# Performance work log

Measured on AMD Instinct MI355X. Metric: run time of the kernel, lower is better.

Reference implementation:

```python
import jax, jax.numpy as jnp
import numpy as np

GRID_SIZE = 5
SPLINE_ORDER = 3
NUM_BASIS = GRID_SIZE + SPLINE_ORDER  # 8


def _make_grid(in_features):
    # efficient-kan style uniform extended grid over [-1, 1]
    h = 2.0 / GRID_SIZE
    g = jnp.arange(-SPLINE_ORDER, GRID_SIZE + SPLINE_ORDER + 1, dtype=jnp.float32) * h - 1.0
    return jnp.broadcast_to(g, (in_features, g.shape[0]))  # [in, 12]


def _b_splines(x, grid):
    # x: [..., in], grid: [in, G]; returns [..., in, NUM_BASIS] via Cox-de Boor
    xe = x[..., None]
    bases = ((xe >= grid[:, :-1]) & (xe < grid[:, 1:])).astype(x.dtype)
    for k in range(1, SPLINE_ORDER + 1):
        left = (xe - grid[:, :-(k + 1)]) / (grid[:, k:-1] - grid[:, :-(k + 1)]) * bases[..., :-1]
        right = (grid[:, k + 1:] - xe) / (grid[:, k + 1:] - grid[:, 1:-k]) * bases[..., 1:]
        bases = left + right
    return bases


def kan_linear(x, bw, sw):
    # bw: [out, in], sw: [out, in, NUM_BASIS]
    base = jnp.matmul(jax.nn.silu(x), bw.T)
    spl = _b_splines(x, _make_grid(bw.shape[1]))
    spline = jnp.einsum('...ik,oik->...o', spl, sw)
    return base + spline


def kan2(x, bw1, sw1, bw2, sw2):
    return kan_linear(kan_linear(x, bw1, sw1), bw2, sw2)


def _att_matrix(q, bw1, sw1, bw2, sw2):
    n, h = q.shape
    pairs = jnp.concatenate([
        jnp.broadcast_to(q[:, None, :], (n, n, h)),
        jnp.broadcast_to(q[None, :, :], (n, n, h)),
    ], axis=-1)  # [n, n, 2h]
    return kan2(pairs, bw1, sw1, bw2, sw2)[..., 0]  # [n, n]


def setup_inputs() -> dict:
    key = jax.random.key(0)
    ks = jax.random.split(key, 32)
    n, h, m = 384, 32, 50

    def rn(k, shape, s=1.0):
        return jax.random.normal(k, shape, dtype=jnp.float32) * s

    inp = {
        'x': rn(ks[0], (n, h)),
        'y': rn(ks[1], (n, h)),
        'target': rn(ks[2], (n, h)),
        'bias': rn(ks[3], (1,), 0.1),
    }
    i = 4
    for pre in ('x', 'y', 't'):
        din = 2 * h
        inp[pre + '1bw'] = rn(ks[i], (m, din), 0.1)
        inp[pre + '1sw'] = rn(ks[i + 1], (m, din, NUM_BASIS), 0.1)
        inp[pre + '2bw'] = rn(ks[i + 2], (1, m), 0.1)
        inp[pre + '2sw'] = rn(ks[i + 3], (1, m, NUM_BASIS), 0.1)
        i += 4
    inp['f1bw'] = rn(ks[i], (m, 3 * h), 0.1)
    inp['f1sw'] = rn(ks[i + 1], (m, 3 * h, NUM_BASIS), 0.1)
    inp['f2bw'] = rn(ks[i + 2], (3, m), 0.1)
    inp['f2sw'] = rn(ks[i + 3], (3, m, NUM_BASIS), 0.1)
    i += 4
    inp['l1bw'] = rn(ks[i], (h, h), 0.1)
    inp['l1sw'] = rn(ks[i + 1], (h, h, NUM_BASIS), 0.1)
    inp['l2bw'] = rn(ks[i + 2], (h, h), 0.1)
    inp['l2sw'] = rn(ks[i + 3], (h, h, NUM_BASIS), 0.1)
    return inp


def reference(x, y, target, bias,
              x1bw, x1sw, x2bw, x2sw,
              y1bw, y1sw, y2bw, y2sw,
              t1bw, t1sw, t2bw, t2sw,
              f1bw, f1sw, f2bw, f2sw,
              l1bw, l1sw, l2bw, l2sw):
    xA = _att_matrix(x, x1bw, x1sw, x2bw, x2sw)
    yA = _att_matrix(y, y1bw, y1sw, y2bw, y2sw)
    tA = _att_matrix(target, t1bw, t1sw, t2bw, t2sw)

    # dynamic modal fusion weights
    feats = jnp.concatenate([x.mean(0, keepdims=True), y.mean(0, keepdims=True),
                             target.mean(0, keepdims=True)], axis=-1)  # [1, 3h]
    w = jax.nn.softmax(kan2(feats, f1bw, f1sw, f2bw, f2sw), axis=-1)[0]  # [3]

    fusion_att = w[0] * xA + w[1] * yA + w[2] * tA + bias
    fusion_att = jax.nn.softmax(fusion_att, axis=-1)
    target_att = jnp.matmul(fusion_att, target)  # dropout is identity at eval
    y1 = jax.nn.relu(kan_linear(target_att, l1bw, l1sw))
    y2 = jax.nn.relu(kan_linear(y1, l2bw, l2sw))
    return y2
```

## Files before the change

kernel.cpp:

```cpp
#include <hip/hip_runtime.h>

#define NN 384
#define HH 32
#define MM 50

__device__ __forceinline__ float fastRcp(float x) { return __builtin_amdgcn_rcpf(x); }

__device__ __forceinline__ void featEval(float x, float& sil, int& kb, float b[4]) {
  sil = x * fastRcp(1.0f + __expf(-x));
  const float u  = (x + 1.0f) * 2.5f;
  const float fu = floorf(u);
  const bool valid = (fu >= -3.0f) && (fu <= 7.0f);
  const float s = valid ? (1.0f / 6.0f) : 0.0f;
  kb = valid ? (int)fu : 100;
  const float tt = u - fu;
  const float t2 = tt * tt, t3 = t2 * tt, omt = 1.0f - tt;
  b[0] = omt * omt * omt * s;
  b[1] = (3.0f * t3 - 6.0f * t2 + 4.0f) * s;
  b[2] = (-3.0f * t3 + 3.0f * t2 + 3.0f * tt + 1.0f) * s;
  b[3] = t3 * s;
}

__device__ __forceinline__ float waveReduce(float v) {
#pragma unroll
  for (int off = 32; off > 0; off >>= 1) v += __shfl_down(v, off);
  return v;
}

__device__ __forceinline__ float dot4(float4 a, float4 b) {
  float r = a.x * b.x;
  r = fmaf(a.y, b.y, r);
  r = fmaf(a.z, b.z, r);
  r = fmaf(a.w, b.w, r);
  return r;
}

__global__ __launch_bounds__(384) void stageA_kernel(
    const float* __restrict__ x, const float* __restrict__ y, const float* __restrict__ tg,
    const float* __restrict__ xbw, const float* __restrict__ xsw,
    const float* __restrict__ ybw, const float* __restrict__ ysw,
    const float* __restrict__ tbw, const float* __restrict__ tsw,
    const float* __restrict__ f1bw, const float* __restrict__ f1sw,
    const float* __restrict__ f2bw, const float* __restrict__ f2sw,
    float* __restrict__ A, float* __restrict__ Bt, float* __restrict__ wout)
{
  const int tid = threadIdx.x;
  const int lane = tid & 63, w = tid >> 6;
  const int i = blockIdx.x;
  const int m = blockIdx.y;
  const int half = blockIdx.z;

  if (i < NN) {
    __shared__ float bas[HH * 8];
    __shared__ float sil[HH];
    const float* q  = (m == 0) ? x   : ((m == 1) ? y   : tg);
    const float* bw = (m == 0) ? xbw : ((m == 1) ? ybw : tbw);
    const float* sw = (m == 0) ? xsw : ((m == 1) ? ysw : tsw);
    const int cb = half * HH;

    if (tid < HH * 8) bas[tid] = 0.0f;
    __syncthreads();
    if (tid < HH) {
      float b[4]; float s; int kb;
      featEval(q[i * HH + tid], s, kb, b);
      sil[tid] = s;
#pragma unroll
      for (int r = 0; r < 4; ++r) {
        const int k = kb + r;
        if ((unsigned)k < 8u) bas[tid * 8 + k] = b[r];
      }
    }
    __syncthreads();

    const float4* bas4 = (const float4*)bas;
    const float4 bb = bas4[lane];
    const float sl = (lane < HH) ? sil[lane] : 0.0f;
#pragma unroll 2
    for (int o = w; o < MM; o += 6) {
      const float4 wv4 = ((const float4*)(sw + ((size_t)(o * 2 * HH + cb) << 3)))[lane];
      const float bwv = (lane < HH) ? bw[o * 2 * HH + cb + lane] : 0.0f;
      float acc = dot4(wv4, bb);
      acc = fmaf(bwv, sl, acc);
      acc = waveReduce(acc);
      if (lane == 0) {
        if (half == 0) A[((size_t)m * NN + i) * MM + o] = acc;
        else           Bt[((size_t)m * MM + o) * NN + i] = acc;
      }
    }
    return;
  }

  if (m != 0 || half != 0) return;
  {
    __shared__ float4 part4[3][8][16];
    __shared__ float sil96[96];
    __shared__ float bas768[96 * 8];
    __shared__ float z1[MM];
    __shared__ float sil2[MM];
    __shared__ float bas400[MM * 8];
    __shared__ float s3[3];

    {
      const int mm = tid >> 7;
      const int sub = tid & 127;
      const int q4 = sub >> 4;
      const int prt = sub & 15;
      const float* src = (mm == 0) ? x : ((mm == 1) ? y : tg);
      const float4* s4 = (const float4*)src;
      float4 a = make_float4(0.f, 0.f, 0.f, 0.f);
      for (int r = prt; r < NN; r += 16) {
        const float4 v = s4[r * 8 + q4];
        a.x += v.x; a.y += v.y; a.z += v.z; a.w += v.w;
      }
      part4[mm][q4][prt] = a;
    }
    for (int idx = tid; idx < 96 * 8; idx += 384) bas768[idx] = 0.0f;
    for (int idx = tid; idx < MM * 8; idx += 384) bas400[idx] = 0.0f;
    __syncthreads();

    if (tid < 96) {
      const int mm = tid >> 5, col = tid & 31;
      const int q4 = col >> 2, comp = col & 3;
      const float* pp = (const float*)&part4[mm][q4][0];
      float v = 0.0f;
#pragma unroll
      for (int prt = 0; prt < 16; ++prt) v += pp[prt * 4 + comp];
      const float fv = v * (1.0f / NN);
      float b[4]; float s; int kb;
      featEval(fv, s, kb, b);
      sil96[tid] = s;
#pragma unroll
      for (int r = 0; r < 4; ++r) {
        const int k = kb + r;
        if ((unsigned)k < 8u) bas768[tid * 8 + k] = b[r];
      }
    }
    __syncthreads();

    {
      const float4* bas4 = (const float4*)bas768;
      for (int o = w; o < MM; o += 6) {
        const float4* sp4 = (const float4*)(f1sw + (size_t)o * (96 * 8));
        float acc = 0.0f;
#pragma unroll
        for (int r = 0; r < 3; ++r)
          acc += dot4(sp4[lane + 64 * r], bas4[lane + 64 * r]);
#pragma unroll
        for (int r = 0; r < 2; ++r) {
          const int e = lane + 64 * r;
          if (e < 96) acc = fmaf(f1bw[o * 96 + e], sil96[e], acc);
        }
        acc = waveReduce(acc);
        if (lane == 0) z1[o] = acc;
      }
    }
    __syncthreads();

    if (tid < MM) {
      float b[4]; float s; int kb;
      featEval(z1[tid], s, kb, b);
      sil2[tid] = s;
#pragma unroll
      for (int r = 0; r < 4; ++r) {
        const int k = kb + r;
        if ((unsigned)k < 8u) bas400[tid * 8 + k] = b[r];
      }
    }
    __syncthreads();

    if (w < 3) {
      const float4* bas4 = (const float4*)bas400;
      const float4* sp4 = (const float4*)(f2sw + (size_t)w * (MM * 8));
      float acc = 0.0f;
#pragma unroll
      for (int r = 0; r < 2; ++r) {
        const int f = lane + 64 * r;
        if (f < MM * 2) acc += dot4(sp4[f], bas4[f]);
      }
      if (lane < MM) acc = fmaf(f2bw[w * MM + lane], sil2[lane], acc);
      acc = waveReduce(acc);
      if (lane == 0) s3[w] = acc;
    }
    __syncthreads();

    if (tid == 0) {
      const float mx = fmaxf(s3[0], fmaxf(s3[1], s3[2]));
      const float e0 = __expf(s3[0] - mx), e1 = __expf(s3[1] - mx), e2 = __expf(s3[2] - mx);
      const float inv = fastRcp(e0 + e1 + e2);
      wout[0] = e0 * inv; wout[1] = e1 * inv; wout[2] = e2 * inv;
    }
  }
}

__global__ __launch_bounds__(384) void score_kernel(
    const float* __restrict__ A, const float* __restrict__ Bt,
    const float* __restrict__ x2bw, const float* __restrict__ y2bw, const float* __restrict__ t2bw,
    const float* __restrict__ x2sw, const float* __restrict__ y2sw, const float* __restrict__ t2sw,
    float* __restrict__ Sp)
{
  __shared__ float sA[MM];
  __shared__ float sBW[MM];
  __shared__ float4 herm[43];
  __shared__ float4 coefC[MM][43];
  const int tid = threadIdx.x;
  const int i = blockIdx.x;
  const int m = blockIdx.y;
  const float* bsrc = (m == 0) ? x2bw : ((m == 1) ? y2bw : t2bw);
  const float* ssrc = (m == 0) ? x2sw : ((m == 1) ? y2sw : t2sw);

  if (tid < MM) {
    sA[tid]  = A[((size_t)m * NN + i) * MM + tid];
    sBW[tid] = bsrc[tid];
  }
  if (tid >= 64 && tid < 64 + 43) {
    const int c = tid - 64;
    float4 h;
    if (c == 0) {
      h = make_float4(0.f, 0.f, 0.f, 0.f);
    } else if (c == 42) {
      h = make_float4(8.2f, 0.4f, 0.f, 0.f);
    } else {
      const float z0 = -8.2f + (float)(c - 1) * 0.4f;
      const float z1 = z0 + 0.4f;
      const float s0 = fastRcp(1.0f + __expf(-z0));
      const float s1 = fastRcp(1.0f + __expf(-z1));
      const float p0 = z0 * s0, p1 = z1 * s1;
      const float m0 = 0.4f * (s0 * (1.0f + z0 * (1.0f - s0)));
      const float m1 = 0.4f * (s1 * (1.0f + z1 * (1.0f - s1)));
      h.x = p0;
      h.y = m0;
      h.z = 3.0f * (p1 - p0) - 2.0f * m0 - m1;
      h.w = 2.0f * (p0 - p1) + m0 + m1;
    }
    herm[c] = h;
  }
  __syncthreads();

  for (int idx = tid; idx < MM * 43; idx += 384) {
    const int k = idx / 43, cc = idx - k * 43;
    const float bwk = sBW[k];
    const float4 H = herm[cc];
    float4 C = make_float4(bwk * H.x, bwk * H.y, bwk * H.z, bwk * H.w);
    if (cc >= 16 && cc <= 26) {
      const int j = cc - 16;
      float p[4];
#pragma unroll
      for (int r = 0; r < 4; ++r) {
        const int pi = j + r - 3;
        p[r] = ((unsigned)pi < 8u) ? ssrc[k * 8 + pi] : 0.0f;
      }
      C.x += (p[0] + 4.0f * p[1] + p[2]) * (1.0f / 6.0f);
      C.y += (p[2] - p[0]) * 0.5f;
      C.z += (p[0] - 2.0f * p[1] + p[2]) * 0.5f;
      C.w += (p[3] - p[0]) * (1.0f / 6.0f) + (p[1] - p[2]) * 0.5f;
    }
    coefC[k][cc] = C;
  }
  __syncthreads();

#define KAN_EVAL(zz, kk, accv)                                          \
  {                                                                     \
    const float z_ = (zz);                                              \
    const float u_ = fmaf(z_, 2.5f, 20.5f);                             \
    const float fu_ = floorf(u_);                                       \
    const float cu_ = fminf(fmaxf(fu_, -1.0f), 41.0f);                  \
    const float t_ = u_ - cu_;                                          \
    const int cc_ = (int)cu_ + 1;                                       \
    const float4 C_ = coefC[kk][cc_];                                   \
    accv += fmaf(t_, fmaf(t_, fmaf(t_, C_.w, C_.z), C_.y), C_.x);       \
  }

  const float* BtBase = Bt + (size_t)m * MM * NN + tid;
  float acc0 = 0.0f, acc1 = 0.0f;
  float za = BtBase[0];
  float zb = BtBase[NN];
  float zc = BtBase[2 * NN];
  float zd = BtBase[3 * NN];
#pragma unroll 5
  for (int k = 0; k < MM; k += 2) {
    float ze = 0.0f, zf = 0.0f;
    if (k + 5 < MM) {
      ze = BtBase[(size_t)(k + 4) * NN];
      zf = BtBase[(size_t)(k + 5) * NN];
    }
    KAN_EVAL(sA[k] + za,     k,     acc0);
    KAN_EVAL(sA[k + 1] + zb, k + 1, acc1);
    za = zc; zb = zd; zc = ze; zd = zf;
  }
#undef KAN_EVAL

  Sp[((size_t)m * NN + i) * NN + tid] = acc0 + acc1;
}

__global__ __launch_bounds__(384) void row_kernel(
    const float* __restrict__ Sp, const float* __restrict__ wv, const float* __restrict__ bias,
    const float* __restrict__ tg,
    const float* __restrict__ l1bw, const float* __restrict__ l1sw,
    const float* __restrict__ l2bw, const float* __restrict__ l2sw,
    float* __restrict__ out)
{
  __shared__ float p[NN];
  __shared__ float redm[6], reds[6];
  __shared__ float part[12][HH];
  __shared__ float ta[HH];
  __shared__ float basF[HH * 8];
  __shared__ float silF[HH];
  __shared__ float y1v[HH];
  const int tid = threadIdx.x;
  const int lane = tid & 63, w = tid >> 6;
  const int i = blockIdx.x;

  float stot = bias[0];
  stot = fmaf(wv[0], Sp[(size_t)i * NN + tid], stot);
  stot = fmaf(wv[1], Sp[((size_t)NN + i) * NN + tid], stot);
  stot = fmaf(wv[2], Sp[((size_t)2 * NN + i) * NN + tid], stot);

  float v = stot;
#pragma unroll
  for (int off = 32; off > 0; off >>= 1) v = fmaxf(v, __shfl_down(v, off));
  if (lane == 0) redm[w] = v;
  __syncthreads();
  float mx = redm[0];
#pragma unroll
  for (int ww = 1; ww < 6; ++ww) mx = fmaxf(mx, redm[ww]);
  const float e = __expf(stot - mx);
  p[tid] = e;
  float sv = e;
#pragma unroll
  for (int off = 32; off > 0; off >>= 1) sv += __shfl_down(sv, off);
  if (lane == 0) reds[w] = sv;
  __syncthreads();
  const float ssum = reds[0] + reds[1] + reds[2] + reds[3] + reds[4] + reds[5];
  const float inv = 1.0f / ssum;

  const int d = tid & 31, g = tid >> 5;
  float acc2 = 0.0f;
  for (int s2 = 0; s2 < 32; ++s2) {
    const int j = g * 32 + s2;
    acc2 = fmaf(p[j], tg[j * HH + d], acc2);
  }
  part[g][d] = acc2;
  if (tid < HH * 8) basF[tid] = 0.0f;
  __syncthreads();
  if (tid < HH) {
    float a = 0.0f;
#pragma unroll
    for (int gg = 0; gg < 12; ++gg) a += part[gg][tid];
    ta[tid] = a * inv;
  }
  __syncthreads();

  if (tid < HH) {
    float b[4]; float s; int kb;
    featEval(ta[tid], s, kb, b);
    silF[tid] = s;
#pragma unroll
    for (int r = 0; r < 4; ++r) {
      const int k = kb + r;
      if ((unsigned)k < 8u) basF[tid * 8 + k] = b[r];
    }
  }
  __syncthreads();
  {
    const float4 bb = ((const float4*)basF)[lane];
    for (int o = w; o < HH; o += 6) {
      const float4* sp4 = (const float4*)(l1sw + ((size_t)o << 8));
      float acc = dot4(sp4[lane], bb);
      if (lane < HH) acc = fmaf(l1bw[o * HH + lane], silF[lane], acc);
      acc = waveReduce(acc);
      if (lane == 0) y1v[o] = fmaxf(acc, 0.0f);
    }
  }
  __syncthreads();
  if (tid < HH * 8) basF[tid] = 0.0f;
  __syncthreads();
  if (tid < HH) {
    float b[4]; float s; int kb;
    featEval(y1v[tid], s, kb, b);
    silF[tid] = s;
#pragma unroll
    for (int r = 0; r < 4; ++r) {
      const int k = kb + r;
      if ((unsigned)k < 8u) basF[tid * 8 + k] = b[r];
    }
  }
  __syncthreads();
  {
    const float4 bb = ((const float4*)basF)[lane];
    for (int o = w; o < HH; o += 6) {
      const float4* sp4 = (const float4*)(l2sw + ((size_t)o << 8));
      float acc = dot4(sp4[lane], bb);
      if (lane < HH) acc = fmaf(l2bw[o * HH + lane], silF[lane], acc);
      acc = waveReduce(acc);
      if (lane == 0) out[i * HH + o] = fmaxf(acc, 0.0f);
    }
  }
}

extern "C" void kernel_launch(void* const* d_in, const int* in_sizes, int n_in,
                              void* d_out, int out_size, void* d_ws, size_t ws_size,
                              hipStream_t stream)
{
  const float* x    = (const float*)d_in[0];
  const float* y    = (const float*)d_in[1];
  const float* tg   = (const float*)d_in[2];
  const float* bias = (const float*)d_in[3];
  const float* x1bw = (const float*)d_in[4];
  const float* x1sw = (const float*)d_in[5];
  const float* x2bw = (const float*)d_in[6];
  const float* x2sw = (const float*)d_in[7];
  const float* y1bw = (const float*)d_in[8];
  const float* y1sw = (const float*)d_in[9];
  const float* y2bw = (const float*)d_in[10];
  const float* y2sw = (const float*)d_in[11];
  const float* t1bw = (const float*)d_in[12];
  const float* t1sw = (const float*)d_in[13];
  const float* t2bw = (const float*)d_in[14];
  const float* t2sw = (const float*)d_in[15];
  const float* f1bw = (const float*)d_in[16];
  const float* f1sw = (const float*)d_in[17];
  const float* f2bw = (const float*)d_in[18];
  const float* f2sw = (const float*)d_in[19];
  const float* l1bw = (const float*)d_in[20];
  const float* l1sw = (const float*)d_in[21];
  const float* l2bw = (const float*)d_in[22];
  const float* l2sw = (const float*)d_in[23];
  float* out = (float*)d_out;

  float* ws = (float*)d_ws;
  float* A  = ws;
  float* Bt = ws + 3 * NN * MM;
  float* Sp = ws + 6 * NN * MM;
  float* wv = Sp + 3 * NN * NN;

  stageA_kernel<<<dim3(NN + 1, 3, 2), 384, 0, stream>>>(
      x, y, tg, x1bw, x1sw, y1bw, y1sw, t1bw, t1sw,
      f1bw, f1sw, f2bw, f2sw, A, Bt, wv);
  score_kernel<<<dim3(NN, 3), 384, 0, stream>>>(A, Bt, x2bw, y2bw, t2bw,
                                                x2sw, y2sw, t2sw, Sp);
  row_kernel<<<NN, 384, 0, stream>>>(Sp, wv, bias, tg, l1bw, l1sw, l2bw, l2sw, out);
}
```

Measured before the change: 46.25 us.

## Pre-transpose first-layer KAN weights so each lane computes one output

Adds a prep kernel that repacks the spline and base weights of the three attention first layers into an output-contiguous float4 layout. Stage A then handles both halves in one block: each of six waves takes one half and a third of the features, and each lane accumulates one output with coalesced loads. This drops the per-output wave shuffle reductions and halves the block count. The cost is an extra kernel launch and a weight transpose that runs on every call.

```diff
diff --git a/kernel.cpp b/kernel.cpp
--- a/kernel.cpp
+++ b/kernel.cpp
@@ -35,62 +35,87 @@
   return r;
 }
 
-__global__ __launch_bounds__(384) void stageA_kernel(
-    const float* __restrict__ x, const float* __restrict__ y, const float* __restrict__ tg,
+__global__ __launch_bounds__(256) void prep_kernel(
     const float* __restrict__ xbw, const float* __restrict__ xsw,
     const float* __restrict__ ybw, const float* __restrict__ ysw,
     const float* __restrict__ tbw, const float* __restrict__ tsw,
+    float4* __restrict__ wt4)
+{
+  const int g = blockIdx.x * 256 + threadIdx.x;
+  if (g >= 3 * 2 * 72 * 50) return;
+  const int o = g % 50;
+  int rem = g / 50;
+  const int e4 = rem % 72;
+  rem /= 72;
+  const int half = rem & 1;
+  const int m = rem >> 1;
+  const float* sw = (m == 0) ? xsw : ((m == 1) ? ysw : tsw);
+  const float* bw = (m == 0) ? xbw : ((m == 1) ? ybw : tbw);
+  float4 v;
+  if (e4 < 64) {
+    v = *(const float4*)(sw + (size_t)o * 512 + half * 256 + e4 * 4);
+  } else {
+    v = *(const float4*)(bw + (size_t)o * 64 + half * 32 + (e4 - 64) * 4);
+  }
+  wt4[((size_t)(m * 2 + half) * 72 + e4) * 50 + o] = v;
+}
+
+__global__ __launch_bounds__(384) void stageA_kernel(
+    const float* __restrict__ x, const float* __restrict__ y, const float* __restrict__ tg,
     const float* __restrict__ f1bw, const float* __restrict__ f1sw,
     const float* __restrict__ f2bw, const float* __restrict__ f2sw,
+    const float4* __restrict__ wt4,
     float* __restrict__ A, float* __restrict__ Bt, float* __restrict__ wout)
 {
   const int tid = threadIdx.x;
   const int lane = tid & 63, w = tid >> 6;
   const int i = blockIdx.x;
   const int m = blockIdx.y;
-  const int half = blockIdx.z;
 
   if (i < NN) {
-    __shared__ float bas[HH * 8];
-    __shared__ float sil[HH];
-    const float* q  = (m == 0) ? x   : ((m == 1) ? y   : tg);
-    const float* bw = (m == 0) ? xbw : ((m == 1) ? ybw : tbw);
-    const float* sw = (m == 0) ? xsw : ((m == 1) ? ysw : tsw);
-    const int cb = half * HH;
-
-    if (tid < HH * 8) bas[tid] = 0.0f;
+    __shared__ float feat[288];
+    __shared__ float psum[2][3][MM + 2];
+    const float* q = (m == 0) ? x : ((m == 1) ? y : tg);
+
+    if (tid < 288) feat[tid] = 0.0f;
     __syncthreads();
     if (tid < HH) {
       float b[4]; float s; int kb;
       featEval(q[i * HH + tid], s, kb, b);
-      sil[tid] = s;
+      feat[256 + tid] = s;
 #pragma unroll
       for (int r = 0; r < 4; ++r) {
         const int k = kb + r;
-        if ((unsigned)k < 8u) bas[tid * 8 + k] = b[r];
-      }
-    }
-    __syncthreads();
-
-    const float4* bas4 = (const float4*)bas;
-    const float4 bb = bas4[lane];
-    const float sl = (lane < HH) ? sil[lane] : 0.0f;
-#pragma unroll 2
-    for (int o = w; o < MM; o += 6) {
-      const float4 wv4 = ((const float4*)(sw + ((size_t)(o * 2 * HH + cb) << 3)))[lane];
-      const float bwv = (lane < HH) ? bw[o * 2 * HH + cb + lane] : 0.0f;
-      float acc = dot4(wv4, bb);
-      acc = fmaf(bwv, sl, acc);
-      acc = waveReduce(acc);
-      if (lane == 0) {
-        if (half == 0) A[((size_t)m * NN + i) * MM + o] = acc;
-        else           Bt[((size_t)m * MM + o) * NN + i] = acc;
-      }
+        if ((unsigned)k < 8u) feat[tid * 8 + k] = b[r];
+      }
+    }
+    __syncthreads();
+
+    const int half = (w >= 3) ? 1 : 0;
+    const int chunk = (w >= 3) ? (w - 3) : w;
+    const float4* feat4 = (const float4*)feat;
+    const float4* wbase = wt4 + (size_t)(m * 2 + half) * 72 * 50;
+    float acc = 0.0f;
+    if (lane < MM) {
+      const int e0 = chunk * 24;
+#pragma unroll 8
+      for (int e4 = e0; e4 < e0 + 24; ++e4) {
+        acc = fmaf(1.0f, dot4(wbase[(size_t)e4 * 50 + lane], feat4[e4]), acc);
+      }
+    }
+    if (lane < MM) psum[half][chunk][lane] = acc;
+    __syncthreads();
+    if (tid < 2 * MM) {
+      const int h = (tid >= MM) ? 1 : 0;
+      const int o = tid - h * MM;
+      const float s = psum[h][0][o] + psum[h][1][o] + psum[h][2][o];
+      if (h == 0) A[((size_t)m * NN + i) * MM + o] = s;
+      else        Bt[((size_t)m * MM + o) * NN + i] = s;
     }
     return;
   }
 
-  if (m != 0 || half != 0) return;
+  if (m != 0) return;
   {
     __shared__ float4 part4[3][8][16];
     __shared__ float sil96[96];
@@ -428,14 +453,16 @@
   float* out = (float*)d_out;
 
   float* ws = (float*)d_ws;
-  float* A  = ws;
-  float* Bt = ws + 3 * NN * MM;
-  float* Sp = ws + 6 * NN * MM;
-  float* wv = Sp + 3 * NN * NN;
-
-  stageA_kernel<<<dim3(NN + 1, 3, 2), 384, 0, stream>>>(
-      x, y, tg, x1bw, x1sw, y1bw, y1sw, t1bw, t1sw,
-      f1bw, f1sw, f2bw, f2sw, A, Bt, wv);
+  float* A   = ws;
+  float* Bt  = ws + 3 * NN * MM;
+  float* Sp  = ws + 6 * NN * MM;
+  float* wv  = Sp + 3 * NN * NN;
+  float4* wt4 = (float4*)(wv + 4);
+
+  prep_kernel<<<(3 * 2 * 72 * 50 + 255) / 256, 256, 0, stream>>>(
+      x1bw, x1sw, y1bw, y1sw, t1bw, t1sw, wt4);
+  stageA_kernel<<<dim3(NN + 1, 3), 384, 0, stream>>>(
+      x, y, tg, f1bw, f1sw, f2bw, f2sw, wt4, A, Bt, wv);
   score_kernel<<<dim3(NN, 3), 384, 0, stream>>>(A, Bt, x2bw, y2bw, t2bw,
                                                 x2sw, y2sw, t2sw, Sp);
   row_kernel<<<NN, 384, 0, stream>>>(Sp, wv, bias, tg, l1bw, l1sw, l2bw, l2sw, out);
```

Measured after the change: 52.68 us. 13.9% more time.

## Fuse score and row kernels, interleave two outputs per wave reduction

Applied to the files above, without the earlier changes.

Merges score_kernel and row_kernel into one kernel, so each block loops over the three modalities, rebuilds the coefficient table in shared memory for each, and accumulates the fused score directly in registers. This removes the Sp intermediate buffer's global write and read plus one kernel launch. The trade-off is fewer blocks (384 instead of 1152) and three serialized coefficient-table builds per block, which can reduce parallelism. Separately, stageA now processes two outputs per wave with interleaved shuffle reductions to raise instruction-level parallelism.

```diff
diff --git a/kernel.cpp b/kernel.cpp
--- a/kernel.cpp
+++ b/kernel.cpp
@@ -75,16 +75,30 @@
     const float4* bas4 = (const float4*)bas;
     const float4 bb = bas4[lane];
     const float sl = (lane < HH) ? sil[lane] : 0.0f;
-#pragma unroll 2
-    for (int o = w; o < MM; o += 6) {
-      const float4 wv4 = ((const float4*)(sw + ((size_t)(o * 2 * HH + cb) << 3)))[lane];
-      const float bwv = (lane < HH) ? bw[o * 2 * HH + cb + lane] : 0.0f;
-      float acc = dot4(wv4, bb);
-      acc = fmaf(bwv, sl, acc);
-      acc = waveReduce(acc);
+    for (int oa = w; oa < MM; oa += 12) {
+      const int ob = oa + 6;
+      const bool hasB = (ob < MM);
+      const float4 wa = ((const float4*)(sw + ((size_t)(oa * 2 * HH + cb) << 3)))[lane];
+      const float4 wb = hasB
+        ? ((const float4*)(sw + ((size_t)(ob * 2 * HH + cb) << 3)))[lane]
+        : make_float4(0.f, 0.f, 0.f, 0.f);
+      const float bwa = (lane < HH) ? bw[oa * 2 * HH + cb + lane] : 0.0f;
+      const float bwb = (hasB && lane < HH) ? bw[ob * 2 * HH + cb + lane] : 0.0f;
+      float accA = fmaf(bwa, sl, dot4(wa, bb));
+      float accB = fmaf(bwb, sl, dot4(wb, bb));
+#pragma unroll
+      for (int off = 32; off > 0; off >>= 1) {
+        accA += __shfl_down(accA, off);
+        accB += __shfl_down(accB, off);
+      }
       if (lane == 0) {
-        if (half == 0) A[((size_t)m * NN + i) * MM + o] = acc;
-        else           Bt[((size_t)m * MM + o) * NN + i] = acc;
+        if (half == 0) {
+          A[((size_t)m * NN + i) * MM + oa] = accA;
+          if (hasB) A[((size_t)m * NN + i) * MM + ob] = accB;
+        } else {
+          Bt[((size_t)m * MM + oa) * NN + i] = accA;
+          if (hasB) Bt[((size_t)m * MM + ob) * NN + i] = accB;
+        }
       }
     }
     return;
@@ -192,28 +206,39 @@
   }
 }
 
-__global__ __launch_bounds__(384) void score_kernel(
+__global__ __launch_bounds__(384) void scoreRow_kernel(
     const float* __restrict__ A, const float* __restrict__ Bt,
     const float* __restrict__ x2bw, const float* __restrict__ y2bw, const float* __restrict__ t2bw,
     const float* __restrict__ x2sw, const float* __restrict__ y2sw, const float* __restrict__ t2sw,
-    float* __restrict__ Sp)
+    const float* __restrict__ wv, const float* __restrict__ bias,
+    const float* __restrict__ tg,
+    const float* __restrict__ l1bw, const float* __restrict__ l1sw,
+    const float* __restrict__ l2bw, const float* __restrict__ l2sw,
+    float* __restrict__ out)
 {
-  __shared__ float sA[MM];
+  __shared__ float sA[3][MM];
   __shared__ float sBW[MM];
   __shared__ float4 herm[43];
   __shared__ float4 coefC[MM][43];
+  __shared__ float swvb[4];
+  __shared__ float p[NN];
+  __shared__ float redm[6], reds[6];
+  __shared__ float part[12][HH];
+  __shared__ float ta[HH];
+  __shared__ float basF[HH * 8];
+  __shared__ float silF[HH];
+  __shared__ float y1v[HH];
+
   const int tid = threadIdx.x;
+  const int lane = tid & 63, w = tid >> 6;
   const int i = blockIdx.x;
-  const int m = blockIdx.y;
-  const float* bsrc = (m == 0) ? x2bw : ((m == 1) ? y2bw : t2bw);
-  const float* ssrc = (m == 0) ? x2sw : ((m == 1) ? y2sw : t2sw);
-
-  if (tid < MM) {
-    sA[tid]  = A[((size_t)m * NN + i) * MM + tid];
-    sBW[tid] = bsrc[tid];
-  }
-  if (tid >= 64 && tid < 64 + 43) {
-    const int c = tid - 64;
+
+  if (tid < 3 * MM) {
+    const int m = tid / MM, k = tid - m * MM;
+    sA[m][k] = A[((size_t)m * NN + i) * MM + k];
+  }
+  if (tid >= 192 && tid < 192 + 43) {
+    const int c = tid - 192;
     float4 h;
     if (c == 0) {
       h = make_float4(0.f, 0.f, 0.f, 0.f);
@@ -234,29 +259,9 @@
     }
     herm[c] = h;
   }
-  __syncthreads();
-
-  for (int idx = tid; idx < MM * 43; idx += 384) {
-    const int k = idx / 43, cc = idx - k * 43;
-    const float bwk = sBW[k];
-    const float4 H = herm[cc];
-    float4 C = make_float4(bwk * H.x, bwk * H.y, bwk * H.z, bwk * H.w);
-    if (cc >= 16 && cc <= 26) {
-      const int j = cc - 16;
-      float p[4];
-#pragma unroll
-      for (int r = 0; r < 4; ++r) {
-        const int pi = j + r - 3;
-        p[r] = ((unsigned)pi < 8u) ? ssrc[k * 8 + pi] : 0.0f;
-      }
-      C.x += (p[0] + 4.0f * p[1] + p[2]) * (1.0f / 6.0f);
-      C.y += (p[2] - p[0]) * 0.5f;
-      C.z += (p[0] - 2.0f * p[1] + p[2]) * 0.5f;
-      C.w += (p[3] - p[0]) * (1.0f / 6.0f) + (p[1] - p[2]) * 0.5f;
-    }
-    coefC[k][cc] = C;
-  }
-  __syncthreads();
+  if (tid == 0) { swvb[0] = wv[0]; swvb[1] = wv[1]; swvb[2] = wv[2]; swvb[3] = bias[0]; }
+
+  float stot;
 
 #define KAN_EVAL(zz, kk, accv)                                          \
   {                                                                     \
@@ -270,50 +275,56 @@
     accv += fmaf(t_, fmaf(t_, fmaf(t_, C_.w, C_.z), C_.y), C_.x);       \
   }
 
-  const float* BtBase = Bt + (size_t)m * MM * NN + tid;
-  float acc0 = 0.0f, acc1 = 0.0f;
-  float za = BtBase[0];
-  float zb = BtBase[NN];
-  float zc = BtBase[2 * NN];
-  float zd = BtBase[3 * NN];
+#pragma unroll 1
+  for (int m = 0; m < 3; ++m) {
+    const float* bsrc = (m == 0) ? x2bw : ((m == 1) ? y2bw : t2bw);
+    const float* ssrc = (m == 0) ? x2sw : ((m == 1) ? y2sw : t2sw);
+    if (tid < MM) sBW[tid] = bsrc[tid];
+    __syncthreads();
+    for (int idx = tid; idx < MM * 43; idx += 384) {
+      const int k = idx / 43, cc = idx - k * 43;
+      const float bwk = sBW[k];
+      const float4 H = herm[cc];
+      float4 C = make_float4(bwk * H.x, bwk * H.y, bwk * H.z, bwk * H.w);
+      if (cc >= 16 && cc <= 26) {
+        const int j = cc - 16;
+        float pw[4];
+#pragma unroll
+        for (int r = 0; r < 4; ++r) {
+          const int pi = j + r - 3;
+          pw[r] = ((unsigned)pi < 8u) ? ssrc[k * 8 + pi] : 0.0f;
+        }
+        C.x += (pw[0] + 4.0f * pw[1] + pw[2]) * (1.0f / 6.0f);
+        C.y += (pw[2] - pw[0]) * 0.5f;
+        C.z += (pw[0] - 2.0f * pw[1] + pw[2]) * 0.5f;
+        C.w += (pw[3] - pw[0]) * (1.0f / 6.0f) + (pw[1] - pw[2]) * 0.5f;
+      }
+      coefC[k][cc] = C;
+    }
+    __syncthreads();
+
+    const float* BtBase = Bt + (size_t)m * MM * NN + tid;
+    float acc0 = 0.0f, acc1 = 0.0f;
+    float za = BtBase[0];
+    float zb = BtBase[NN];
+    float zc = BtBase[2 * NN];
+    float zd = BtBase[3 * NN];
 #pragma unroll 5
-  for (int k = 0; k < MM; k += 2) {
-    float ze = 0.0f, zf = 0.0f;
-    if (k + 5 < MM) {
-      ze = BtBase[(size_t)(k + 4) * NN];
-      zf = BtBase[(size_t)(k + 5) * NN];
-    }
-    KAN_EVAL(sA[k] + za,     k,     acc0);
-    KAN_EVAL(sA[k + 1] + zb, k + 1, acc1);
-    za = zc; zb = zd; zc = ze; zd = zf;
+    for (int k = 0; k < MM; k += 2) {
+      float ze = 0.0f, zf = 0.0f;
+      if (k + 5 < MM) {
+        ze = BtBase[(size_t)(k + 4) * NN];
+        zf = BtBase[(size_t)(k + 5) * NN];
+      }
+      KAN_EVAL(sA[m][k] + za,     k,     acc0);
+      KAN_EVAL(sA[m][k + 1] + zb, k + 1, acc1);
+      za = zc; zb = zd; zc = ze; zd = zf;
+    }
+    const float accm = acc0 + acc1;
+    if (m == 0) stot = fmaf(swvb[0], accm, swvb[3]);
+    else        stot = fmaf(swvb[m], accm, stot);
   }
 #undef KAN_EVAL
-
-  Sp[((size_t)m * NN + i) * NN + tid] = acc0 + acc1;
-}
-
-__global__ __launch_bounds__(384) void row_kernel(
-    const float* __restrict__ Sp, const float* __restrict__ wv, const float* __restrict__ bias,
-    const float* __restrict__ tg,
-    const float* __restrict__ l1bw, const float* __restrict__ l1sw,
-    const float* __restrict__ l2bw, const float* __restrict__ l2sw,
-    float* __restrict__ out)
-{
-  __shared__ float p[NN];
-  __shared__ float redm[6], reds[6];
-  __shared__ float part[12][HH];
-  __shared__ float ta[HH];
-  __shared__ float basF[HH * 8];
-  __shared__ float silF[HH];
-  __shared__ float y1v[HH];
-  const int tid = threadIdx.x;
-  const int lane = tid & 63, w = tid >> 6;
-  const int i = blockIdx.x;
-
-  float stot = bias[0];
-  stot = fmaf(wv[0], Sp[(size_t)i * NN + tid], stot);
-  stot = fmaf(wv[1], Sp[((size_t)NN + i) * NN + tid], stot);
-  stot = fmaf(wv[2], Sp[((size_t)2 * NN + i) * NN + tid], stot);
 
   float v = stot;
 #pragma unroll
@@ -430,13 +441,12 @@
   float* ws = (float*)d_ws;
   float* A  = ws;
   float* Bt = ws + 3 * NN * MM;
-  float* Sp = ws + 6 * NN * MM;
-  float* wv = Sp + 3 * NN * NN;
+  float* wv = ws + 6 * NN * MM;
 
   stageA_kernel<<<dim3(NN + 1, 3, 2), 384, 0, stream>>>(
       x, y, tg, x1bw, x1sw, y1bw, y1sw, t1bw, t1sw,
       f1bw, f1sw, f2bw, f2sw, A, Bt, wv);
-  score_kernel<<<dim3(NN, 3), 384, 0, stream>>>(A, Bt, x2bw, y2bw, t2bw,
-                                                x2sw, y2sw, t2sw, Sp);
-  row_kernel<<<NN, 384, 0, stream>>>(Sp, wv, bias, tg, l1bw, l1sw, l2bw, l2sw, out);
-}
+  scoreRow_kernel<<<NN, 384, 0, stream>>>(
+      A, Bt, x2bw, y2bw, t2bw, x2sw, y2sw, t2sw,
+      wv, bias, tg, l1bw, l1sw, l2bw, l2sw, out);
+}
```

After: 50.04 us. 8.2% more time.

## Tile stage A over six rows per block with spline weights cached in LDS

Applied to the files above, without the earlier changes.

Stage A now processes six query rows per block instead of one. The block loads the modality's spline and base weight slice into padded shared memory once, and each thread computes one (row, output) dot product serially, exploiting the sparse 4-of-8 basis support. The grid shrinks from 385 to 65 blocks per modality/half. This cuts redundant global weight loads and wave reductions, in exchange for fewer blocks, a large LDS footprint and lower parallelism per block.

```diff
diff --git a/kernel.cpp b/kernel.cpp
--- a/kernel.cpp
+++ b/kernel.cpp
@@ -46,46 +46,73 @@
 {
   const int tid = threadIdx.x;
   const int lane = tid & 63, w = tid >> 6;
-  const int i = blockIdx.x;
+  const int bi = blockIdx.x;
   const int m = blockIdx.y;
   const int half = blockIdx.z;
 
-  if (i < NN) {
-    __shared__ float bas[HH * 8];
-    __shared__ float sil[HH];
+  if (bi < 64) {
+    __shared__ float WL[MM][257];
+    __shared__ float bwL[MM][33];
+    __shared__ float silL[6][HH];
+    __shared__ float bL[6][HH][4];
+    __shared__ int   kbL[6][HH];
+    const int i0 = bi * 6;
     const float* q  = (m == 0) ? x   : ((m == 1) ? y   : tg);
     const float* bw = (m == 0) ? xbw : ((m == 1) ? ybw : tbw);
     const float* sw = (m == 0) ? xsw : ((m == 1) ? ysw : tsw);
     const int cb = half * HH;
 
-    if (tid < HH * 8) bas[tid] = 0.0f;
-    __syncthreads();
-    if (tid < HH) {
+    for (int idx = tid; idx < MM * 64; idx += 384) {
+      const int o = idx >> 6, j4 = idx & 63;
+      const float4 v = *(const float4*)(sw + (size_t)o * 512 + half * 256 + (j4 << 2));
+      float* dst = &WL[o][j4 << 2];
+      dst[0] = v.x; dst[1] = v.y; dst[2] = v.z; dst[3] = v.w;
+    }
+    for (int idx = tid; idx < MM * HH; idx += 384) {
+      const int o = idx >> 5, d = idx & 31;
+      bwL[o][d] = bw[o * 64 + cb + d];
+    }
+    if (tid < 6 * HH) {
+      const int r = tid >> 5, d = tid & 31;
       float b[4]; float s; int kb;
-      featEval(q[i * HH + tid], s, kb, b);
-      sil[tid] = s;
-#pragma unroll
-      for (int r = 0; r < 4; ++r) {
-        const int k = kb + r;
-        if ((unsigned)k < 8u) bas[tid * 8 + k] = b[r];
-      }
-    }
-    __syncthreads();
-
-    const float4* bas4 = (const float4*)bas;
-    const float4 bb = bas4[lane];
-    const float sl = (lane < HH) ? sil[lane] : 0.0f;
+      featEval(q[(i0 + r) * HH + d], s, kb, b);
+      silL[r][d] = s;
+      kbL[r][d] = kb;
+      bL[r][d][0] = b[0]; bL[r][d][1] = b[1]; bL[r][d][2] = b[2]; bL[r][d][3] = b[3];
+    }
+    __syncthreads();
+
+    if (tid < 6 * MM) {
+      const int r = tid / MM, o = tid - r * MM;
+      const int i = i0 + r;
+      float acc0 = 0.0f, acc1 = 0.0f;
 #pragma unroll 2
-    for (int o = w; o < MM; o += 6) {
-      const float4 wv4 = ((const float4*)(sw + ((size_t)(o * 2 * HH + cb) << 3)))[lane];
-      const float bwv = (lane < HH) ? bw[o * 2 * HH + cb + lane] : 0.0f;
-      float acc = dot4(wv4, bb);
-      acc = fmaf(bwv, sl, acc);
-      acc = waveReduce(acc);
-      if (lane == 0) {
-        if (half == 0) A[((size_t)m * NN + i) * MM + o] = acc;
-        else           Bt[((size_t)m * MM + o) * NN + i] = acc;
-      }
+      for (int d = 0; d < HH; d += 2) {
+        {
+          acc0 = fmaf(silL[r][d], bwL[o][d], acc0);
+          const int kb = kbL[r][d];
+          const float* wrow = &WL[o][d * 8];
+#pragma unroll
+          for (int rr = 0; rr < 4; ++rr) {
+            const int k = kb + rr;
+            if ((unsigned)k < 8u) acc0 = fmaf(bL[r][d][rr], wrow[k], acc0);
+          }
+        }
+        {
+          const int d1 = d + 1;
+          acc1 = fmaf(silL[r][d1], bwL[o][d1], acc1);
+          const int kb = kbL[r][d1];
+          const float* wrow = &WL[o][d1 * 8];
+#pragma unroll
+          for (int rr = 0; rr < 4; ++rr) {
+            const int k = kb + rr;
+            if ((unsigned)k < 8u) acc1 = fmaf(bL[r][d1][rr], wrow[k], acc1);
+          }
+        }
+      }
+      const float acc = acc0 + acc1;
+      if (half == 0) A[((size_t)m * NN + i) * MM + o] = acc;
+      else           Bt[((size_t)m * MM + o) * NN + i] = acc;
     }
     return;
   }
@@ -433,7 +460,7 @@
   float* Sp = ws + 6 * NN * MM;
   float* wv = Sp + 3 * NN * NN;
 
-  stageA_kernel<<<dim3(NN + 1, 3, 2), 384, 0, stream>>>(
+  stageA_kernel<<<dim3(65, 3, 2), 384, 0, stream>>>(
       x, y, tg, x1bw, x1sw, y1bw, y1sw, t1bw, t1sw,
       f1bw, f1sw, f2bw, f2sw, A, Bt, wv);
   score_kernel<<<dim3(NN, 3), 384, 0, stream>>>(A, Bt, x2bw, y2bw, t2bw,
```

Measured after the change: 52.11 us. 12.7% more time.
